# Kernel tuning notes

Hardware: AMD Instinct MI355X
Metric: run time of the kernel (lower is better)

The kernel has to match this reference:

```python
import jax, jax.numpy as jnp
import numpy as np

T, B, P, Q, WW, WF, C = 7, 512, 200, 64, 64, 256, 10
N = B * P
SIGMA = 0.1


def _lin(key, fin, fout):
    kw, kb = jax.random.split(key)
    s = 1.0 / np.sqrt(fin)
    return (jax.random.uniform(kw, (fin, fout), minval=-s, maxval=s),
            jax.random.uniform(kb, (fout,), minval=-s, maxval=s))


def setup_inputs() -> dict:
    key = jax.random.key(0)
    ks = jax.random.split(key, 9)
    diagms = jax.random.normal(ks[0], (T, N, 2), dtype=jnp.float32)
    # repeat_interleave(arange(B), counts): equal-sized segments of P points
    seg_ids = jnp.tile(jnp.repeat(jnp.arange(B, dtype=jnp.int32), P), (T, 1))
    theta = jax.random.normal(ks[1], (Q, 2), dtype=jnp.float32)
    w1, b1 = _lin(ks[2], 2, WW)
    w2, b2 = _lin(ks[3], WW, WW)
    w3, b3 = _lin(ks[4], WW, 1)
    r1, rb1 = _lin(ks[5], T * Q, WF)
    r2, rb2 = _lin(ks[6], WF, WF)
    r3, rb3 = _lin(ks[7], WF, C)
    return dict(diagms=diagms, seg_ids=seg_ids, theta=theta,
                w1=w1, b1=b1, w2=w2, b2=b2, w3=w3, b3=b3,
                r1=r1, rb1=rb1, r2=r2, rb2=rb2, r3=r3, rb3=rb3)


def reference(diagms, seg_ids, theta, w1, b1, w2, b2, w3, b3,
              r1, rb1, r2, rb2, r3, rb3):
    # gaussian kernel: exp(-||x - theta||^2 / (2 sigma^2)), cdist expanded
    diff = diagms[:, :, None, :] - theta[None, None, :, :]      # [T,N,Q,2]
    rep = jnp.exp(-jnp.sum(diff * diff, axis=-1) / (2.0 * SIGMA ** 2))  # [T,N,Q]
    # weight MLP on raw (birth,death) coords, shared across types
    h = jax.nn.relu(diagms @ w1 + b1)
    h = jax.nn.relu(h @ w2 + b2)
    w = jax.nn.sigmoid(h @ w3 + b3)                              # [T,N,1]
    rep = w * rep
    # global_mean_pool per diagram type via segment sum
    def pool(r, s):
        sums = jax.ops.segment_sum(r, s, num_segments=B)         # [B,Q]
        cnts = jax.ops.segment_sum(jnp.ones((r.shape[0],), r.dtype), s,
                                   num_segments=B)
        return sums / jnp.maximum(cnts, 1.0)[:, None]
    pooled = jax.vmap(pool)(rep, seg_ids)                        # [T,B,Q]
    topo = jnp.transpose(pooled, (1, 0, 2)).reshape(B, T * Q)    # cat over types
    # final MLP rho
    z = jax.nn.relu(topo @ r1 + rb1)
    z = jax.nn.relu(z @ r2 + rb2)
    return z @ r3 + rb3                                          # [B,C]
```

## Files before the change

kernel.cpp:

```cpp
#include <hip/hip_runtime.h>
#include <hip/hip_bf16.h>
#include <math.h>

#define TT 7
#define BB 512
#define PP 200
#define QQ 64
#define WWH 64
#define WF 256
#define CC 10
#define NN (BB * PP)
#define TQ (TT * QQ)

typedef __attribute__((ext_vector_type(8))) short short8;
typedef __attribute__((ext_vector_type(4))) float f32x4;

static __device__ __forceinline__ unsigned short f2bf(float f) {
    __hip_bfloat16 b = __float2bfloat16(f);
    return *reinterpret_cast<unsigned short*>(&b);
}

#define NEG50_OVER_LN2 (-72.13475204444817f)

__global__ __launch_bounds__(256, 3) void fused_weight_pool_kernel(
    const float* __restrict__ diagms,
    const float* __restrict__ theta,
    const float* __restrict__ w1,
    const float* __restrict__ b1,
    const float* __restrict__ w2,
    const float* __restrict__ b2,
    const float* __restrict__ w3,
    const float* __restrict__ b3,
    float* __restrict__ pooled)
{
    __shared__ unsigned short Hl[256 * 64];
    __shared__ unsigned short W2T[64 * 64];
    __shared__ float px[256];
    __shared__ float py[256];
    __shared__ float wv[256];
    __shared__ float part[4][QQ];

    const int bid  = blockIdx.x;
    const int t    = bid >> 9;
    const int b    = bid & (BB - 1);
    const int tid  = threadIdx.x;
    const int lane = tid & 63;
    const int wvx  = tid >> 6;

    {
        const int n  = tid & 63;
        const int j0 = (tid >> 6) * 16;
#pragma unroll
        for (int jj = 0; jj < 16; ++jj) {
            const int j = j0 + jj;
            const float v = w2[j * WWH + n];
            const int off = n * 64 + ((((j >> 3) ^ (n & 7))) << 3) + (j & 7);
            W2T[off] = f2bf(v);
        }
    }

    {
        const int base = t * NN + b * PP;
        int gidx = base + tid;
        if (gidx > TT * NN - 1) gidx = TT * NN - 1;
        const float2 d = reinterpret_cast<const float2*>(diagms)[gidx];
        const float x = d.x, y = d.y;
        px[tid] = x;
        py[tid] = y;
        uint4* Hrow = reinterpret_cast<uint4*>(Hl);
#pragma unroll
        for (int i = 0; i < 8; ++i) {
            unsigned int pk[4];
#pragma unroll
            for (int e = 0; e < 4; ++e) {
                const int j = i * 8 + 2 * e;
                const float h0 = fmaxf(fmaf(x, w1[j],     fmaf(y, w1[WWH + j],     b1[j])),     0.0f);
                const float h1 = fmaxf(fmaf(x, w1[j + 1], fmaf(y, w1[WWH + j + 1], b1[j + 1])), 0.0f);
                pk[e] = (unsigned int)f2bf(h0) | ((unsigned int)f2bf(h1) << 16);
            }
            uint4 v; v.x = pk[0]; v.y = pk[1]; v.z = pk[2]; v.w = pk[3];
            Hrow[tid * 8 + (i ^ (tid & 7))] = v;
        }
    }

    __syncthreads();

    {
        float b2v[4], w3v[4];
#pragma unroll
        for (int nt = 0; nt < 4; ++nt) {
            b2v[nt] = b2[nt * 16 + (lane & 15)];
            w3v[nt] = w3[nt * 16 + (lane & 15)];
        }
        const float b3s = b3[0];

        short8 bfr[2][4];
#pragma unroll
        for (int s = 0; s < 2; ++s) {
#pragma unroll
            for (int nt = 0; nt < 4; ++nt) {
                const int n = nt * 16 + (lane & 15);
                const int slot = ((lane >> 4) + s * 4) ^ (lane & 7);
                bfr[s][nt] = reinterpret_cast<const short8*>(W2T)[n * 8 + slot];
            }
        }

        const int wave_p0 = wvx * 64;

#pragma unroll 1
        for (int m = 0; m < 4; ++m) {
            f32x4 acc[4];
#pragma unroll
            for (int nt = 0; nt < 4; ++nt) acc[nt] = (f32x4){0.f, 0.f, 0.f, 0.f};

#pragma unroll
            for (int s = 0; s < 2; ++s) {
                const int p = wave_p0 + m * 16 + (lane & 15);
                const int slot = ((lane >> 4) + s * 4) ^ (lane & 7);
                const short8 af = reinterpret_cast<const short8*>(Hl)[p * 8 + slot];
#pragma unroll
                for (int nt = 0; nt < 4; ++nt) {
                    acc[nt] = __builtin_amdgcn_mfma_f32_16x16x32_bf16(af, bfr[s][nt], acc[nt], 0, 0, 0);
                }
            }

            float sum0 = 0.f, sum1 = 0.f, sum2 = 0.f, sum3 = 0.f;
#pragma unroll
            for (int nt = 0; nt < 4; ++nt) {
                sum0 = fmaf(fmaxf(acc[nt][0] + b2v[nt], 0.f), w3v[nt], sum0);
                sum1 = fmaf(fmaxf(acc[nt][1] + b2v[nt], 0.f), w3v[nt], sum1);
                sum2 = fmaf(fmaxf(acc[nt][2] + b2v[nt], 0.f), w3v[nt], sum2);
                sum3 = fmaf(fmaxf(acc[nt][3] + b2v[nt], 0.f), w3v[nt], sum3);
            }
#pragma unroll
            for (int off = 1; off < 16; off <<= 1) {
                sum0 += __shfl_xor(sum0, off, 64);
                sum1 += __shfl_xor(sum1, off, 64);
                sum2 += __shfl_xor(sum2, off, 64);
                sum3 += __shfl_xor(sum3, off, 64);
            }
            const int r_sel = lane & 15;
            if (r_sel < 4) {
                const float sv = (r_sel == 0) ? sum0 : (r_sel == 1) ? sum1
                               : (r_sel == 2) ? sum2 : sum3;
                const float wa = sv + b3s;
                const int prow = wave_p0 + m * 16 + ((lane >> 4) << 2) + r_sel;
                wv[prow] = 1.0f / (1.0f + __expf(-wa));
            }
        }
    }

    __syncthreads();

    {
        const int q = tid & (QQ - 1);
        const int g = tid >> 6;
        const float2 th = reinterpret_cast<const float2*>(theta)[q];
        const float tx = th.x;
        const float ty = th.y;

        float acc = 0.0f;
        const int p0 = g * (PP / 4);
#pragma unroll 5
        for (int p = p0; p < p0 + PP / 4; ++p) {
            const float dx = px[p] - tx;
            const float dy = py[p] - ty;
            acc = fmaf(wv[p], exp2f(fmaf(dx, dx, dy * dy) * NEG50_OVER_LN2), acc);
        }
        part[g][q] = acc;
    }
    __syncthreads();

    if (tid < QQ) {
        const float s = (part[0][tid] + part[1][tid]) + (part[2][tid] + part[3][tid]);
        pooled[b * TQ + t * QQ + tid] = s * (1.0f / (float)PP);
    }
}

#define K3_ROWS 2
__global__ __launch_bounds__(1024, 4) void rho_kernel(
    const float* __restrict__ pooled,
    const float* __restrict__ r1,
    const float* __restrict__ rb1,
    const float* __restrict__ r2,
    const float* __restrict__ rb2,
    const float* __restrict__ r3,
    const float* __restrict__ rb3,
    float* __restrict__ out)
{
    const int b0  = blockIdx.x * K3_ROWS;
    const int tid = threadIdx.x;
    const int k   = tid & (WF - 1);
    const int g   = tid >> 8;

    __shared__ float tp[K3_ROWS * TQ];
    __shared__ float z1[K3_ROWS][WF];
    __shared__ float z2[K3_ROWS][WF];
    __shared__ float part[4][K3_ROWS][WF];
    __shared__ float red[8][CC];

    if (tid < K3_ROWS * TQ) tp[tid] = pooled[(size_t)b0 * TQ + tid];
    __syncthreads();

    {
        float acc0 = 0.0f, acc1 = 0.0f;
        const float* r1c = r1 + k;
        const int ibase = g * (TQ / 4);
        float rv0[8], rv1[8];
#pragma unroll
        for (int e = 0; e < 8; ++e) rv0[e] = r1c[(ibase + e) * WF];
#pragma unroll 1
        for (int i0 = ibase; i0 < ibase + TQ / 4; i0 += 16) {
#pragma unroll
            for (int e = 0; e < 8; ++e) rv1[e] = r1c[(i0 + 8 + e) * WF];
#pragma unroll
            for (int e = 0; e < 8; ++e) {
                acc0 = fmaf(tp[i0 + e],      rv0[e], acc0);
                acc1 = fmaf(tp[TQ + i0 + e], rv0[e], acc1);
            }
            if (i0 + 16 < ibase + TQ / 4) {
#pragma unroll
                for (int e = 0; e < 8; ++e) rv0[e] = r1c[(i0 + 16 + e) * WF];
            }
#pragma unroll
            for (int e = 0; e < 8; ++e) {
                acc0 = fmaf(tp[i0 + 8 + e],      rv1[e], acc0);
                acc1 = fmaf(tp[TQ + i0 + 8 + e], rv1[e], acc1);
            }
        }
        part[g][0][k] = acc0;
        part[g][1][k] = acc1;
    }
    __syncthreads();
    if (tid < 2 * WF) {
        const int r = tid >> 8;
        const int kk = tid & (WF - 1);
        z1[r][kk] = fmaxf(part[0][r][kk] + part[1][r][kk] +
                          part[2][r][kk] + part[3][r][kk] + rb1[kk], 0.0f);
    }
    __syncthreads();

    {
        float acc0 = 0.0f, acc1 = 0.0f;
        const float* r2c = r2 + k;
        const int ibase = g * (WF / 4);
        float rv0[8], rv1[8];
#pragma unroll
        for (int e = 0; e < 8; ++e) rv0[e] = r2c[(ibase + e) * WF];
#pragma unroll 1
        for (int i0 = ibase; i0 < ibase + WF / 4; i0 += 16) {
#pragma unroll
            for (int e = 0; e < 8; ++e) rv1[e] = r2c[(i0 + 8 + e) * WF];
#pragma unroll
            for (int e = 0; e < 8; ++e) {
                acc0 = fmaf(z1[0][i0 + e], rv0[e], acc0);
                acc1 = fmaf(z1[1][i0 + e], rv0[e], acc1);
            }
            if (i0 + 16 < ibase + WF / 4) {
#pragma unroll
                for (int e = 0; e < 8; ++e) rv0[e] = r2c[(i0 + 16 + e) * WF];
            }
#pragma unroll
            for (int e = 0; e < 8; ++e) {
                acc0 = fmaf(z1[0][i0 + 8 + e], rv1[e], acc0);
                acc1 = fmaf(z1[1][i0 + 8 + e], rv1[e], acc1);
            }
        }
        part[g][0][k] = acc0;
        part[g][1][k] = acc1;
    }
    __syncthreads();
    if (tid < 2 * WF) {
        const int r = tid >> 8;
        const int kk = tid & (WF - 1);
        z2[r][kk] = fmaxf(part[0][r][kk] + part[1][r][kk] +
                          part[2][r][kk] + part[3][r][kk] + rb2[kk], 0.0f);
    }
    __syncthreads();

    if (tid < 512) {
        const int r    = tid >> 8;
        const int kk   = tid & (WF - 1);
        const int lane = tid & 63;
        const int wvi  = tid >> 6;
        const float z = z2[r][kk];
        float p[CC];
#pragma unroll
        for (int c = 0; c < CC; ++c) p[c] = z * r3[kk * CC + c];
#pragma unroll
        for (int off = 32; off >= 1; off >>= 1) {
#pragma unroll
            for (int c = 0; c < CC; ++c) p[c] += __shfl_xor(p[c], off, 64);
        }
        if (lane == 0) {
#pragma unroll
            for (int c = 0; c < CC; ++c) red[wvi][c] = p[c];
        }
    }
    __syncthreads();
    if (tid < K3_ROWS * CC) {
        const int r = tid / CC;
        const int c = tid % CC;
        out[(size_t)(b0 + r) * CC + c] =
            red[r * 4 + 0][c] + red[r * 4 + 1][c] +
            red[r * 4 + 2][c] + red[r * 4 + 3][c] + rb3[c];
    }
}

extern "C" void kernel_launch(void* const* d_in, const int* in_sizes, int n_in,
                              void* d_out, int out_size, void* d_ws, size_t ws_size,
                              hipStream_t stream)
{
    const float* diagms = (const float*)d_in[0];
    const float* theta  = (const float*)d_in[2];
    const float* w1     = (const float*)d_in[3];
    const float* b1     = (const float*)d_in[4];
    const float* w2     = (const float*)d_in[5];
    const float* b2     = (const float*)d_in[6];
    const float* w3     = (const float*)d_in[7];
    const float* b3     = (const float*)d_in[8];
    const float* r1     = (const float*)d_in[9];
    const float* rb1    = (const float*)d_in[10];
    const float* r2     = (const float*)d_in[11];
    const float* rb2    = (const float*)d_in[12];
    const float* r3     = (const float*)d_in[13];
    const float* rb3    = (const float*)d_in[14];
    float* out = (float*)d_out;

    float* pooled = (float*)d_ws;

    fused_weight_pool_kernel<<<TT * BB, 256, 0, stream>>>(
        diagms, theta, w1, b1, w2, b2, w3, b3, pooled);

    rho_kernel<<<BB / K3_ROWS, 1024, 0, stream>>>(
        pooled, r1, rb1, r2, rb2, r3, rb3, out);
}
```

Baseline: 135.9 us.

## Split fused weight/pool kernel into dense per-point weight kernel and pool kernel

The fused kernel handled one (type, batch) segment of 200 points with 256 threads, leaving 56 threads idle in the MLP stage. It is now two kernels. The first computes the sigmoid point weights densely over all points, with every thread busy, and writes them to a global buffer. The second reloads coordinates and weights, packed in shared memory as float4, and does the Gaussian pooling. This trades the wasted lanes for a global round trip of the weights (about 2.9 MB), an extra kernel launch and a second read of diagms.

```diff
diff --git a/kernel.cpp b/kernel.cpp
--- a/kernel.cpp
+++ b/kernel.cpp
@@ -22,30 +22,22 @@
 
 #define NEG50_OVER_LN2 (-72.13475204444817f)
 
-__global__ __launch_bounds__(256, 3) void fused_weight_pool_kernel(
+__global__ __launch_bounds__(256, 4) void point_weight_kernel(
     const float* __restrict__ diagms,
-    const float* __restrict__ theta,
     const float* __restrict__ w1,
     const float* __restrict__ b1,
     const float* __restrict__ w2,
     const float* __restrict__ b2,
     const float* __restrict__ w3,
     const float* __restrict__ b3,
-    float* __restrict__ pooled)
+    float* __restrict__ w_out)
 {
     __shared__ unsigned short Hl[256 * 64];
     __shared__ unsigned short W2T[64 * 64];
-    __shared__ float px[256];
-    __shared__ float py[256];
-    __shared__ float wv[256];
-    __shared__ float part[4][QQ];
-
-    const int bid  = blockIdx.x;
-    const int t    = bid >> 9;
-    const int b    = bid & (BB - 1);
+
     const int tid  = threadIdx.x;
     const int lane = tid & 63;
-    const int wvx  = tid >> 6;
+    const int wv   = tid >> 6;
 
     {
         const int n  = tid & 63;
@@ -60,13 +52,9 @@
     }
 
     {
-        const int base = t * NN + b * PP;
-        int gidx = base + tid;
-        if (gidx > TT * NN - 1) gidx = TT * NN - 1;
-        const float2 d = reinterpret_cast<const float2*>(diagms)[gidx];
+        const int p = tid;
+        const float2 d = reinterpret_cast<const float2*>(diagms)[(size_t)blockIdx.x * 256 + p];
         const float x = d.x, y = d.y;
-        px[tid] = x;
-        py[tid] = y;
         uint4* Hrow = reinterpret_cast<uint4*>(Hl);
 #pragma unroll
         for (int i = 0; i < 8; ++i) {
@@ -79,96 +67,121 @@
                 pk[e] = (unsigned int)f2bf(h0) | ((unsigned int)f2bf(h1) << 16);
             }
             uint4 v; v.x = pk[0]; v.y = pk[1]; v.z = pk[2]; v.w = pk[3];
-            Hrow[tid * 8 + (i ^ (tid & 7))] = v;
-        }
-    }
-
-    __syncthreads();
-
-    {
-        float b2v[4], w3v[4];
+            Hrow[p * 8 + (i ^ (p & 7))] = v;
+        }
+    }
+
+    __syncthreads();
+
+    float b2v[4], w3v[4];
+#pragma unroll
+    for (int nt = 0; nt < 4; ++nt) {
+        b2v[nt] = b2[nt * 16 + (lane & 15)];
+        w3v[nt] = w3[nt * 16 + (lane & 15)];
+    }
+    const float b3s = b3[0];
+
+    short8 bf[2][4];
+#pragma unroll
+    for (int s = 0; s < 2; ++s) {
 #pragma unroll
         for (int nt = 0; nt < 4; ++nt) {
-            b2v[nt] = b2[nt * 16 + (lane & 15)];
-            w3v[nt] = w3[nt * 16 + (lane & 15)];
-        }
-        const float b3s = b3[0];
-
-        short8 bfr[2][4];
+            const int n = nt * 16 + (lane & 15);
+            const int slot = ((lane >> 4) + s * 4) ^ (lane & 7);
+            bf[s][nt] = reinterpret_cast<const short8*>(W2T)[n * 8 + slot];
+        }
+    }
+
+    const int wave_p0 = wv * 64;
+    const size_t out_base = (size_t)blockIdx.x * 256;
+
+#pragma unroll 1
+    for (int m = 0; m < 4; ++m) {
+        f32x4 acc[4];
+#pragma unroll
+        for (int nt = 0; nt < 4; ++nt) acc[nt] = (f32x4){0.f, 0.f, 0.f, 0.f};
+
 #pragma unroll
         for (int s = 0; s < 2; ++s) {
+            const int p = wave_p0 + m * 16 + (lane & 15);
+            const int slot = ((lane >> 4) + s * 4) ^ (lane & 7);
+            const short8 af = reinterpret_cast<const short8*>(Hl)[p * 8 + slot];
 #pragma unroll
             for (int nt = 0; nt < 4; ++nt) {
-                const int n = nt * 16 + (lane & 15);
-                const int slot = ((lane >> 4) + s * 4) ^ (lane & 7);
-                bfr[s][nt] = reinterpret_cast<const short8*>(W2T)[n * 8 + slot];
-            }
-        }
-
-        const int wave_p0 = wvx * 64;
-
-#pragma unroll 1
-        for (int m = 0; m < 4; ++m) {
-            f32x4 acc[4];
-#pragma unroll
-            for (int nt = 0; nt < 4; ++nt) acc[nt] = (f32x4){0.f, 0.f, 0.f, 0.f};
-
-#pragma unroll
-            for (int s = 0; s < 2; ++s) {
-                const int p = wave_p0 + m * 16 + (lane & 15);
-                const int slot = ((lane >> 4) + s * 4) ^ (lane & 7);
-                const short8 af = reinterpret_cast<const short8*>(Hl)[p * 8 + slot];
-#pragma unroll
-                for (int nt = 0; nt < 4; ++nt) {
-                    acc[nt] = __builtin_amdgcn_mfma_f32_16x16x32_bf16(af, bfr[s][nt], acc[nt], 0, 0, 0);
-                }
-            }
-
-            float sum0 = 0.f, sum1 = 0.f, sum2 = 0.f, sum3 = 0.f;
-#pragma unroll
-            for (int nt = 0; nt < 4; ++nt) {
-                sum0 = fmaf(fmaxf(acc[nt][0] + b2v[nt], 0.f), w3v[nt], sum0);
-                sum1 = fmaf(fmaxf(acc[nt][1] + b2v[nt], 0.f), w3v[nt], sum1);
-                sum2 = fmaf(fmaxf(acc[nt][2] + b2v[nt], 0.f), w3v[nt], sum2);
-                sum3 = fmaf(fmaxf(acc[nt][3] + b2v[nt], 0.f), w3v[nt], sum3);
-            }
-#pragma unroll
-            for (int off = 1; off < 16; off <<= 1) {
-                sum0 += __shfl_xor(sum0, off, 64);
-                sum1 += __shfl_xor(sum1, off, 64);
-                sum2 += __shfl_xor(sum2, off, 64);
-                sum3 += __shfl_xor(sum3, off, 64);
-            }
-            const int r_sel = lane & 15;
-            if (r_sel < 4) {
-                const float sv = (r_sel == 0) ? sum0 : (r_sel == 1) ? sum1
-                               : (r_sel == 2) ? sum2 : sum3;
-                const float wa = sv + b3s;
-                const int prow = wave_p0 + m * 16 + ((lane >> 4) << 2) + r_sel;
-                wv[prow] = 1.0f / (1.0f + __expf(-wa));
-            }
-        }
-    }
-
-    __syncthreads();
-
-    {
-        const int q = tid & (QQ - 1);
-        const int g = tid >> 6;
-        const float2 th = reinterpret_cast<const float2*>(theta)[q];
-        const float tx = th.x;
-        const float ty = th.y;
-
-        float acc = 0.0f;
-        const int p0 = g * (PP / 4);
+                acc[nt] = __builtin_amdgcn_mfma_f32_16x16x32_bf16(af, bf[s][nt], acc[nt], 0, 0, 0);
+            }
+        }
+
+        float sum0 = 0.f, sum1 = 0.f, sum2 = 0.f, sum3 = 0.f;
+#pragma unroll
+        for (int nt = 0; nt < 4; ++nt) {
+            sum0 = fmaf(fmaxf(acc[nt][0] + b2v[nt], 0.f), w3v[nt], sum0);
+            sum1 = fmaf(fmaxf(acc[nt][1] + b2v[nt], 0.f), w3v[nt], sum1);
+            sum2 = fmaf(fmaxf(acc[nt][2] + b2v[nt], 0.f), w3v[nt], sum2);
+            sum3 = fmaf(fmaxf(acc[nt][3] + b2v[nt], 0.f), w3v[nt], sum3);
+        }
+#pragma unroll
+        for (int off = 1; off < 16; off <<= 1) {
+            sum0 += __shfl_xor(sum0, off, 64);
+            sum1 += __shfl_xor(sum1, off, 64);
+            sum2 += __shfl_xor(sum2, off, 64);
+            sum3 += __shfl_xor(sum3, off, 64);
+        }
+        const int r_sel = lane & 15;
+        if (r_sel < 4) {
+            const float sv = (r_sel == 0) ? sum0 : (r_sel == 1) ? sum1
+                           : (r_sel == 2) ? sum2 : sum3;
+            const float wa = sv + b3s;
+            const float wsig = 1.0f / (1.0f + __expf(-wa));
+            const int prow = wave_p0 + m * 16 + ((lane >> 4) << 2) + r_sel;
+            w_out[out_base + prow] = wsig;
+        }
+    }
+}
+
+__global__ __launch_bounds__(256) void rep_pool_kernel(
+    const float* __restrict__ diagms,
+    const float* __restrict__ theta,
+    const float* __restrict__ w_in,
+    float* __restrict__ pooled)
+{
+    const int bid = blockIdx.x;
+    const int t = bid >> 9;
+    const int b = bid & (BB - 1);
+    const int tid = threadIdx.x;
+
+    __shared__ float4 pxyw[PP];
+
+    if (tid < PP) {
+        const int n = t * NN + b * PP + tid;
+        const float2 d = reinterpret_cast<const float2*>(diagms)[n];
+        float4 v;
+        v.x = d.x;
+        v.y = d.y;
+        v.z = w_in[n];
+        v.w = 0.0f;
+        pxyw[tid] = v;
+    }
+    __syncthreads();
+
+    const int q = tid & (QQ - 1);
+    const int g = tid >> 6;
+    const float2 th = reinterpret_cast<const float2*>(theta)[q];
+    const float tx = th.x;
+    const float ty = th.y;
+
+    float acc = 0.0f;
+    const int p0 = g * (PP / 4);
 #pragma unroll 5
-        for (int p = p0; p < p0 + PP / 4; ++p) {
-            const float dx = px[p] - tx;
-            const float dy = py[p] - ty;
-            acc = fmaf(wv[p], exp2f(fmaf(dx, dx, dy * dy) * NEG50_OVER_LN2), acc);
-        }
-        part[g][q] = acc;
-    }
+    for (int p = p0; p < p0 + PP / 4; ++p) {
+        const float4 v = pxyw[p];
+        const float dx = v.x - tx;
+        const float dy = v.y - ty;
+        acc = fmaf(v.z, exp2f(fmaf(dx, dx, dy * dy) * NEG50_OVER_LN2), acc);
+    }
+
+    __shared__ float part[4][QQ];
+    part[g][q] = acc;
     __syncthreads();
 
     if (tid < QQ) {
@@ -327,10 +340,15 @@
     const float* rb3    = (const float*)d_in[14];
     float* out = (float*)d_out;
 
-    float* pooled = (float*)d_ws;
-
-    fused_weight_pool_kernel<<<TT * BB, 256, 0, stream>>>(
-        diagms, theta, w1, b1, w2, b2, w3, b3, pooled);
+    float* w_buf  = (float*)d_ws;
+    float* pooled = w_buf + (size_t)TT * NN;
+
+    const int total = TT * NN;
+
+    point_weight_kernel<<<total / 256, 256, 0, stream>>>(
+        diagms, w1, b1, w2, b2, w3, b3, w_buf);
+
+    rep_pool_kernel<<<TT * BB, 256, 0, stream>>>(diagms, theta, w_buf, pooled);
 
     rho_kernel<<<BB / K3_ROWS, 1024, 0, stream>>>(
         pooled, r1, rb1, r2, rb2, r3, rb3, out);
```

Result: faster. 127.9 us (-5.9%).
